# Optimization experiments

Hardware: AMD Instinct MI355X
Metric: run time of the kernel (lower is better)

The kernel has to match this reference:

```python
import jax, jax.numpy as jnp
import numpy as np

N = 16384      # total points
B = 8          # point clouds in batch
PER = N // B   # points per cloud (batch ids sorted in blocks)
M = 4096       # sampled centers (ratio 0.25, strided sampler -> batch-aligned)
K = 64         # max_num_neighbors
R = 0.25       # ball-query radius
C_IN = 128
HID = 256
C_OUT = 256


def setup_inputs() -> dict:
    key = jax.random.key(0)
    k1, k2, k3, k4, k5 = jax.random.split(key, 5)
    x = jax.random.normal(k1, (N, C_IN), dtype=jnp.float32)
    pos = jax.random.uniform(k2, (N, 3), dtype=jnp.float32)  # unit cube
    batch = jnp.repeat(jnp.arange(B, dtype=jnp.int32), PER)  # sorted block batch ids
    lframes = jax.random.normal(k3, (N, 3, 3), dtype=jnp.float32)
    W1 = jax.random.normal(k4, (2 * C_IN + 3, HID), dtype=jnp.float32) * 0.05
    b1 = jnp.zeros((HID,), dtype=jnp.float32)
    W2 = jax.random.normal(k5, (HID, C_OUT), dtype=jnp.float32) * 0.05
    b2 = jnp.zeros((C_OUT,), dtype=jnp.float32)
    return {"x": x, "pos": pos, "batch": batch, "lframes": lframes,
            "W1": W1, "b1": b1, "W2": W2, "b2": b2}


def _ball_query(pos, batch, idx):
    """radius(pos, pos[idx], R, batch, batch[idx], max_num_neighbors=K).
    Returns fixed-size neighbor indices [M, K] + validity mask [M, K]."""
    pos_c = pos[idx]                                  # [M, 3]
    # squared distances via gemm trick (avoid [M, N, 3] broadcast)
    d2 = ((pos_c ** 2).sum(-1)[:, None]
          + (pos ** 2).sum(-1)[None, :]
          - 2.0 * pos_c @ pos.T)                      # [M, N]
    valid = (d2 <= R * R) & (batch[idx][:, None] == batch[None, :])
    score = jnp.where(valid, -d2, -jnp.inf)
    vals, nbr = jax.lax.top_k(score, K)               # K nearest within ball
    return nbr, jnp.isfinite(vals)


def reference(x, pos, batch, lframes, W1, b1, W2, b2):
    # center sampler: strided subsample (batch-aligned since batch is block-sorted)
    idx = jnp.arange(0, N, N // M)                    # [M]
    nbr, vmask = _ball_query(pos, batch, idx)         # [M, K]

    pos_dst = pos[idx]                                # [M, 3]
    x_dst = x[idx]                                    # [M, C_IN]
    lframes_dst = lframes[idx]                        # [M, 3, 3]

    # EdgeConv: per-edge message MLP([x_src, x_dst, lframe_dst @ (pos_src - pos_dst)])
    rel = pos[nbr] - pos_dst[:, None, :]              # [M, K, 3]
    rel_loc = jnp.einsum('mij,mkj->mki', lframes_dst, rel)  # rotate into dst frame
    feats = jnp.concatenate([
        x[nbr],                                        # [M, K, C_IN]
        jnp.broadcast_to(x_dst[:, None, :], (M, K, C_IN)),
        rel_loc,
    ], axis=-1)                                        # [M, K, 2*C_IN+3]

    h = jax.nn.relu(feats @ W1 + b1)                   # [M, K, HID]
    msg = h @ W2 + b2                                  # [M, K, C_OUT]

    # masked max aggregation over valid neighbors
    msg = jnp.where(vmask[..., None], msg, -jnp.inf)
    out = msg.max(axis=1)                              # [M, C_OUT]
    out = jnp.where(jnp.isfinite(out), out, 0.0)
    return out, pos_dst, batch[idx], lframes_dst
```

## Files before the change

### kernel.cpp

```cpp
#include <hip/hip_runtime.h>
#include <hip/hip_bf16.h>

#define N_PTS 16384
#define PER   2048
#define M_CTR 4096
#define KNB   64
#define C_IN  128
#define HID   256
#define C_OUT 256

typedef unsigned short u16;
typedef unsigned int u32;
typedef __attribute__((ext_vector_type(8))) short s8v;
typedef __attribute__((ext_vector_type(4))) float f4v;
typedef __attribute__((ext_vector_type(4))) unsigned int u4v;

static __device__ __forceinline__ u16 f2bf(float f) {
    union { float f; unsigned int i; } v; v.f = f;
    unsigned int r = v.i + 0x7FFFu + ((v.i >> 16) & 1u);
    return (u16)(r >> 16);
}

__global__ __launch_bounds__(256) void work_kernel(
        const float* __restrict__ pos, int* __restrict__ nbr, int* __restrict__ cnt,
        const float* __restrict__ W1, const float* __restrict__ W2,
        u16* __restrict__ W2T,
        const float* __restrict__ x, const float* __restrict__ b1,
        u16* __restrict__ u_out, float* __restrict__ v_out) {
    __shared__ char arena[64 * 136 * 2];
    int blk = blockIdx.x, tid = threadIdx.x;

    if (blk < M_CTR) {
        float* cd2 = (float*)arena;
        int*   cidx = (int*)(arena + 4096);
        __shared__ int s_n;
        int m = blk;

        if (m < 256) {
            int gid = m * 256 + tid;
            int cc = gid >> 8, k = gid & 255;
            W2T[gid] = f2bf(W2[k * 256 + cc]);
        }

        int c = m * 4;
        int base = (m >> 9) << 11;
        int ln = tid & 63;
        if (tid == 0) s_n = 0;
        __syncthreads();
        float cx = pos[c * 3 + 0], cy = pos[c * 3 + 1], cz = pos[c * 3 + 2];
        float A = __fadd_rn(__fadd_rn(__fmul_rn(cx, cx), __fmul_rn(cy, cy)), __fmul_rn(cz, cz));
        float c2x = __fmul_rn(2.0f, cx);
        float c2y = __fmul_rn(2.0f, cy);
        float c2z = __fmul_rn(2.0f, cz);
        for (int s = 0; s < 8; ++s) {
            int j = base + tid + (s << 8);
            float px = pos[j * 3 + 0], py = pos[j * 3 + 1], pz = pos[j * 3 + 2];
            float B = __fadd_rn(__fadd_rn(__fmul_rn(px, px), __fmul_rn(py, py)), __fmul_rn(pz, pz));
            float C = __fmaf_rn(c2z, pz, __fmaf_rn(c2y, py, __fmul_rn(c2x, px)));
            float d2 = __fsub_rn(__fadd_rn(A, B), C);
            bool hit = (d2 <= 0.0625f);
            unsigned long long mk = __ballot(hit);
            int nb = __popcll(mk & ((1ull << ln) - 1ull));
            int tot = __popcll(mk);
            int bidx = 0;
            if (ln == 0 && tot) bidx = atomicAdd(&s_n, tot);
            bidx = __shfl(bidx, 0, 64);
            if (hit) {
                int a = bidx + nb;
                if (a < 1024) { cd2[a] = d2; cidx[a] = j; }
            }
        }
        __syncthreads();
        int V = s_n < 1024 ? s_n : 1024;
        if (V <= KNB) {
            if (tid < KNB) nbr[m * KNB + tid] = (tid < V) ? cidx[tid] : c;
            if (tid == 0) cnt[m] = V;
        } else {
            for (int e = tid; e < V; e += 256) {
                float de = cd2[e]; int ie = cidx[e];
                int rank = 0;
                for (int q = 0; q < V; ++q) {
                    float dq = cd2[q];
                    rank += (dq < de) || (dq == de && cidx[q] < ie);
                }
                if (rank < KNB) nbr[m * KNB + rank] = cidx[e];
            }
            if (tid == 0) cnt[m] = KNB;
        }
    } else {
        u16* x_lds = (u16*)arena;
        int blk2 = blk - M_CTR;
        int mode = blk2 >= 256 ? 1 : 0;
        int bb = mode ? blk2 - 256 : blk2;
        const float* W1x = W1 + (mode ? 128 * 256 : 0);
        {
            int r = tid >> 2, q = tid & 3;
            int xrow = bb * 64 + r;
            if (mode) xrow *= 4;
            const float* xp = x + xrow * C_IN + q * 32;
            u16* dst = x_lds + r * 136 + q * 32;
            for (int i = 0; i < 8; ++i) {
                f4v f = *(const f4v*)(xp + i * 4);
                dst[i * 4 + 0] = f2bf(f[0]);
                dst[i * 4 + 1] = f2bf(f[1]);
                dst[i * 4 + 2] = f2bf(f[2]);
                dst[i * 4 + 3] = f2bf(f[3]);
            }
        }
        __syncthreads();
        int lane = tid & 63, w = tid >> 6;
        int quad = lane >> 4, l16 = lane & 15;
        int cb = w * 64;
        f4v acc[4][4] = {};
        for (int k0 = 0; k0 < 128; k0 += 32) {
            s8v a[4], b[4];
            #pragma unroll
            for (int ct = 0; ct < 4; ++ct) {
                int col = cb + ct * 16 + l16;
                const float* wp = W1x + (k0 + quad * 8) * 256 + col;
                union { u4v v4; s8v s8; } pk;
                #pragma unroll
                for (int d = 0; d < 4; ++d) {
                    u16 lo = f2bf(wp[(2 * d) * 256]);
                    u16 hi = f2bf(wp[(2 * d + 1) * 256]);
                    pk.v4[d] = ((u32)hi << 16) | lo;
                }
                b[ct] = pk.s8;
            }
            #pragma unroll
            for (int rt = 0; rt < 4; ++rt)
                a[rt] = *(const s8v*)&x_lds[(rt * 16 + l16) * 136 + k0 + quad * 8];
            #pragma unroll
            for (int rt = 0; rt < 4; ++rt)
                #pragma unroll
                for (int ct = 0; ct < 4; ++ct)
                    acc[rt][ct] = __builtin_amdgcn_mfma_f32_16x16x32_bf16(a[rt], b[ct], acc[rt][ct], 0, 0, 0);
        }
        for (int rt = 0; rt < 4; ++rt)
            for (int ct = 0; ct < 4; ++ct)
                for (int g = 0; g < 4; ++g) {
                    int row = rt * 16 + quad * 4 + g;
                    int col = cb + ct * 16 + l16;
                    float val = acc[rt][ct][g];
                    int orow = bb * 64 + row;
                    if (mode == 0) u_out[orow * 256 + col] = f2bf(val);
                    else           v_out[orow * 256 + col] = val + b1[col];
                }
    }
}

__global__ __launch_bounds__(512, 2) void edge_kernel(
        const u16* __restrict__ u, const float* __restrict__ v,
        const u16* __restrict__ W2T, const float* __restrict__ W1,
        const float* __restrict__ b2, const float* __restrict__ pos,
        const float* __restrict__ lframes, const int* __restrict__ batch,
        const int* __restrict__ nbrg, const int* __restrict__ cnt,
        float* __restrict__ out0, float* __restrict__ out_pos,
        float* __restrict__ out_batch, float* __restrict__ out_lf) {
    __shared__ u16   h_lds[128 * 264];
    __shared__ float v_lds[2][2][256];
    __shared__ float w1c_lds[768];
    __shared__ f4v   relc_lds[2][2][64];
    __shared__ u16   nbr_lds[2][2][64];

    int blk = blockIdx.x, tid = threadIdx.x;
    int m0 = ((blk & 7) << 9) | ((blk >> 3) << 3);

    int lane = tid & 63, w = tid >> 6;
    int quad = lane >> 4, l16 = lane & 15;
    int cb = (w & 3) * 64;
    int rbase = (w >> 2) * 64;
    int gsel = w >> 2;

    for (int i = tid; i < 768; i += 512) w1c_lds[i] = W1[65536 + i];
    if (tid < 128) {
        int g = tid >> 6, t = tid & 63;
        int mm = m0 + g, cc = mm * 4;
        int j = nbrg[mm * KNB + t];
        nbr_lds[0][g][t] = (u16)j;
        float rx = pos[j * 3 + 0] - pos[cc * 3 + 0];
        float ry = pos[j * 3 + 1] - pos[cc * 3 + 1];
        float rz = pos[j * 3 + 2] - pos[cc * 3 + 2];
        const float* lf = lframes + cc * 9;
        f4v r;
        r[0] = lf[0] * rx + lf[1] * ry + lf[2] * rz;
        r[1] = lf[3] * rx + lf[4] * ry + lf[5] * rz;
        r[2] = lf[6] * rx + lf[7] * ry + lf[8] * rz;
        r[3] = 0.0f;
        relc_lds[0][g][t] = r;
    }
    v_lds[0][tid >> 8][tid & 255] = v[(m0 + (tid >> 8)) * 256 + (tid & 255)];
    if (tid >= 256 && tid < 384) {
        int g = (tid - 256) >> 4, t = tid & 15;
        int mm = m0 + g, cc = mm * 4;
        if (t < 3)            out_pos[mm * 3 + t] = pos[cc * 3 + t];
        else if (t == 3)      out_batch[mm] = (float)batch[cc];
        else if (t < 13)      out_lf[mm * 9 + (t - 4)] = lframes[cc * 9 + (t - 4)];
    }

    int co = (tid & 31) * 8;
    int rs = tid >> 5;
    int cv_cur = cnt[m0 + gsel];
    __syncthreads();

    int cv_next = 0;
    for (int p = 0; p < 4; ++p) {
        int pb = p & 1;
        #pragma unroll
        for (int g = 0; g < 2; ++g) {
            f4v vq0 = *(const f4v*)&v_lds[pb][g][co];
            f4v vq1 = *(const f4v*)&v_lds[pb][g][co + 4];
            f4v wa0 = *(const f4v*)&w1c_lds[co],       wa1 = *(const f4v*)&w1c_lds[co + 4];
            f4v wb0 = *(const f4v*)&w1c_lds[256 + co], wb1 = *(const f4v*)&w1c_lds[256 + co + 4];
            f4v wc0 = *(const f4v*)&w1c_lds[512 + co], wc1 = *(const f4v*)&w1c_lds[512 + co + 4];
            #pragma unroll
            for (int i2 = 0; i2 < 4; ++i2) {
                int rl = rs + i2 * 16;
                int row = g * 64 + rl;
                int j = (int)nbr_lds[pb][g][rl];
                u4v uu = *(const u4v*)(u + j * 256 + co);
                f4v r = relc_lds[pb][g][rl];
                float p8[8];
                #pragma unroll
                for (int e = 0; e < 8; ++e) {
                    u32 bits = (e & 1) ? (uu[e >> 1] & 0xFFFF0000u) : (uu[e >> 1] << 16);
                    float va = (e < 4) ? vq0[e] : vq1[e - 4];
                    float a0 = (e < 4) ? wa0[e] : wa1[e - 4];
                    float b0 = (e < 4) ? wb0[e] : wb1[e - 4];
                    float c0 = (e < 4) ? wc0[e] : wc1[e - 4];
                    float pre = fmaf(r[0], a0, fmaf(r[1], b0, fmaf(r[2], c0,
                                  va + __uint_as_float(bits))));
                    p8[e] = fmaxf(pre, 0.0f);
                }
                u4v pk;
                #pragma unroll
                for (int d = 0; d < 4; ++d)
                    pk[d] = __builtin_amdgcn_perm(__float_as_uint(p8[2 * d + 1]),
                                                  __float_as_uint(p8[2 * d]), 0x07060302u);
                *(u4v*)&h_lds[row * 264 + co] = pk;
            }
        }
        if (p < 3) {
            int nb = pb ^ 1;
            int mbase = m0 + (p + 1) * 2;
            cv_next = cnt[mbase + gsel];
            if (tid < 128) {
                int g = tid >> 6, t = tid & 63;
                int mm = mbase + g, cc = mm * 4;
                int j = nbrg[mm * KNB + t];
                nbr_lds[nb][g][t] = (u16)j;
                float rx = pos[j * 3 + 0] - pos[cc * 3 + 0];
                float ry = pos[j * 3 + 1] - pos[cc * 3 + 1];
                float rz = pos[j * 3 + 2] - pos[cc * 3 + 2];
                const float* lf = lframes + cc * 9;
                f4v r;
                r[0] = lf[0] * rx + lf[1] * ry + lf[2] * rz;
                r[1] = lf[3] * rx + lf[4] * ry + lf[5] * rz;
                r[2] = lf[6] * rx + lf[7] * ry + lf[8] * rz;
                r[3] = 0.0f;
                relc_lds[nb][g][t] = r;
            }
            v_lds[nb][tid >> 8][tid & 255] = v[(mbase + (tid >> 8)) * 256 + (tid & 255)];
        }
        __syncthreads();

        f4v acc[4][4] = {};
        for (int k0 = 0; k0 < 256; k0 += 32) {
            s8v a[4], b[4];
            #pragma unroll
            for (int rt = 0; rt < 4; ++rt)
                a[rt] = *(const s8v*)&h_lds[(rbase + rt * 16 + l16) * 264 + k0 + quad * 8];
            #pragma unroll
            for (int ct = 0; ct < 4; ++ct)
                b[ct] = *(const s8v*)(W2T + (cb + ct * 16 + l16) * 256 + k0 + quad * 8);
            #pragma unroll
            for (int rt = 0; rt < 4; ++rt)
                #pragma unroll
                for (int ct = 0; ct < 4; ++ct)
                    acc[rt][ct] = __builtin_amdgcn_mfma_f32_16x16x32_bf16(a[rt], b[ct], acc[rt][ct], 0, 0, 0);
        }
        int mout = m0 + p * 2 + gsel;
        #pragma unroll
        for (int ct = 0; ct < 4; ++ct) {
            float mx = -__builtin_inff();
            #pragma unroll
            for (int rt = 0; rt < 4; ++rt)
                #pragma unroll
                for (int g = 0; g < 4; ++g) {
                    int row = rt * 16 + quad * 4 + g;
                    float val = acc[rt][ct][g];
                    if (row < cv_cur) mx = fmaxf(mx, val);
                }
            mx = fmaxf(mx, __shfl_xor(mx, 16, 64));
            mx = fmaxf(mx, __shfl_xor(mx, 32, 64));
            if (lane < 16)
                out0[mout * 256 + cb + ct * 16 + l16] = mx + b2[cb + ct * 16 + l16];
        }
        cv_cur = cv_next;
        __syncthreads();
    }
}

extern "C" void kernel_launch(void* const* d_in, const int* in_sizes, int n_in,
                              void* d_out, int out_size, void* d_ws, size_t ws_size,
                              hipStream_t stream) {
    const float* x       = (const float*)d_in[0];
    const float* pos     = (const float*)d_in[1];
    const int*   batch   = (const int*)d_in[2];
    const float* lframes = (const float*)d_in[3];
    const float* W1      = (const float*)d_in[4];
    const float* b1      = (const float*)d_in[5];
    const float* W2      = (const float*)d_in[6];
    const float* b2      = (const float*)d_in[7];

    float* out       = (float*)d_out;
    float* out_pos   = out + M_CTR * 256;
    float* out_batch = out_pos + M_CTR * 3;
    float* out_lf    = out_batch + M_CTR;

    char* ws = (char*)d_ws;
    u16*   u_ws = (u16*)(ws);
    float* v_ws = (float*)(ws + 8388608);
    u16*   W2T  = (u16*)(ws + 12713984);
    int*   nbr  = (int*)(ws + 12845056);
    int*   cntp = (int*)(ws + 13893632);

    hipLaunchKernelGGL(work_kernel, dim3(M_CTR + 320), dim3(256), 0, stream,
                       pos, nbr, cntp, W1, W2, W2T, x, b1, u_ws, v_ws);
    hipLaunchKernelGGL(edge_kernel, dim3(512), dim3(512), 0, stream,
                       u_ws, v_ws, W2T, W1, b2, pos, lframes, batch, nbr, cntp,
                       out, out_pos, out_batch, out_lf);
}
```

Baseline: 202.5 us.

## Run ball query with one wavefront per center and packed sort keys

The ball query moves from one 256-thread block per center to one 64-lane wavefront per center, four centers per block. Block-level atomics and __syncthreads are replaced by a per-wave running count from ballot/popcount. Distance and index are packed into one 64-bit orderable key, so the rank sort does a single compare per pair. This cuts the grid size, shared-memory atomics and barriers. In exchange, each wave scans 2048 points serially and the quadratic ranking runs over only 64 lanes instead of 256.

```diff
diff --git a/kernel.cpp b/kernel.cpp
--- a/kernel.cpp
+++ b/kernel.cpp
@@ -11,6 +11,7 @@
 
 typedef unsigned short u16;
 typedef unsigned int u32;
+typedef unsigned long long u64;
 typedef __attribute__((ext_vector_type(8))) short s8v;
 typedef __attribute__((ext_vector_type(4))) float f4v;
 typedef __attribute__((ext_vector_type(4))) unsigned int u4v;
@@ -19,6 +20,11 @@
     union { float f; unsigned int i; } v; v.f = f;
     unsigned int r = v.i + 0x7FFFu + ((v.i >> 16) & 1u);
     return (u16)(r >> 16);
+}
+
+static __device__ __forceinline__ u32 fkey(float f) {
+    u32 b = __float_as_uint(f);
+    return b ^ ((u32)((int)b >> 31) | 0x80000000u);
 }
 
 __global__ __launch_bounds__(256) void work_kernel(
@@ -27,69 +33,61 @@
         u16* __restrict__ W2T,
         const float* __restrict__ x, const float* __restrict__ b1,
         u16* __restrict__ u_out, float* __restrict__ v_out) {
-    __shared__ char arena[64 * 136 * 2];
+    __shared__ char arena[32768];
     int blk = blockIdx.x, tid = threadIdx.x;
 
-    if (blk < M_CTR) {
-        float* cd2 = (float*)arena;
-        int*   cidx = (int*)(arena + 4096);
-        __shared__ int s_n;
-        int m = blk;
-
-        if (m < 256) {
-            int gid = m * 256 + tid;
+    if (blk < 1024) {
+        if (blk < 256) {
+            int gid = blk * 256 + tid;
             int cc = gid >> 8, k = gid & 255;
             W2T[gid] = f2bf(W2[k * 256 + cc]);
         }
-
+        int w = tid >> 6, ln = tid & 63;
+        int m = blk * 4 + w;
         int c = m * 4;
         int base = (m >> 9) << 11;
-        int ln = tid & 63;
-        if (tid == 0) s_n = 0;
-        __syncthreads();
+        u64* cand = (u64*)arena + w * 1024;
+
         float cx = pos[c * 3 + 0], cy = pos[c * 3 + 1], cz = pos[c * 3 + 2];
         float A = __fadd_rn(__fadd_rn(__fmul_rn(cx, cx), __fmul_rn(cy, cy)), __fmul_rn(cz, cz));
         float c2x = __fmul_rn(2.0f, cx);
         float c2y = __fmul_rn(2.0f, cy);
         float c2z = __fmul_rn(2.0f, cz);
-        for (int s = 0; s < 8; ++s) {
-            int j = base + tid + (s << 8);
+        int count = 0;
+        #pragma unroll 4
+        for (int s = 0; s < 32; ++s) {
+            int j = base + ln + (s << 6);
             float px = pos[j * 3 + 0], py = pos[j * 3 + 1], pz = pos[j * 3 + 2];
             float B = __fadd_rn(__fadd_rn(__fmul_rn(px, px), __fmul_rn(py, py)), __fmul_rn(pz, pz));
             float C = __fmaf_rn(c2z, pz, __fmaf_rn(c2y, py, __fmul_rn(c2x, px)));
             float d2 = __fsub_rn(__fadd_rn(A, B), C);
             bool hit = (d2 <= 0.0625f);
-            unsigned long long mk = __ballot(hit);
-            int nb = __popcll(mk & ((1ull << ln) - 1ull));
-            int tot = __popcll(mk);
-            int bidx = 0;
-            if (ln == 0 && tot) bidx = atomicAdd(&s_n, tot);
-            bidx = __shfl(bidx, 0, 64);
+            u64 mk = __ballot(hit);
             if (hit) {
-                int a = bidx + nb;
-                if (a < 1024) { cd2[a] = d2; cidx[a] = j; }
-            }
-        }
-        __syncthreads();
-        int V = s_n < 1024 ? s_n : 1024;
+                int a = count + __popcll(mk & ((1ull << ln) - 1ull));
+                if (a < 1024)
+                    cand[a] = (((u64)fkey(d2)) << 32) | (u32)j;
+            }
+            count += __popcll(mk);
+        }
+        __builtin_amdgcn_wave_barrier();
+        int V = count < 1024 ? count : 1024;
         if (V <= KNB) {
-            if (tid < KNB) nbr[m * KNB + tid] = (tid < V) ? cidx[tid] : c;
-            if (tid == 0) cnt[m] = V;
+            nbr[m * KNB + ln] = (ln < V) ? (int)(cand[ln] & 0xFFFFFFFFu) : c;
+            if (ln == 0) cnt[m] = V;
         } else {
-            for (int e = tid; e < V; e += 256) {
-                float de = cd2[e]; int ie = cidx[e];
+            if (ln == 0) cnt[m] = KNB;
+            for (int e = ln; e < V; e += 64) {
+                u64 ke = cand[e];
                 int rank = 0;
-                for (int q = 0; q < V; ++q) {
-                    float dq = cd2[q];
-                    rank += (dq < de) || (dq == de && cidx[q] < ie);
-                }
-                if (rank < KNB) nbr[m * KNB + rank] = cidx[e];
-            }
-            if (tid == 0) cnt[m] = KNB;
+                for (int q = 0; q < V; ++q)
+                    rank += (cand[q] < ke);
+                if (rank < KNB) nbr[m * KNB + rank] = (int)(ke & 0xFFFFFFFFu);
+            }
         }
     } else {
         u16* x_lds = (u16*)arena;
-        int blk2 = blk - M_CTR;
+        int blk2 = blk - 1024;
         int mode = blk2 >= 256 ? 1 : 0;
         int bb = mode ? blk2 - 256 : blk2;
         const float* W1x = W1 + (mode ? 128 * 256 : 0);
@@ -325,7 +323,7 @@
     int*   nbr  = (int*)(ws + 12845056);
     int*   cntp = (int*)(ws + 13893632);
 
-    hipLaunchKernelGGL(work_kernel, dim3(M_CTR + 320), dim3(256), 0, stream,
+    hipLaunchKernelGGL(work_kernel, dim3(1024 + 320), dim3(256), 0, stream,
                        pos, nbr, cntp, W1, W2, W2T, x, b1, u_ws, v_ws);
     hipLaunchKernelGGL(edge_kernel, dim3(512), dim3(512), 0, stream,
                        u_ws, v_ws, W2T, W1, b2, pos, lframes, batch, nbr, cntp,
```

Result: faster. 186.8 us (-7.7%).
